# Kernel tuning notes

Measured on AMD Instinct MI355X. Metric: run time of the kernel, lower is better.

Reference implementation:

```python
import jax, jax.numpy as jnp
import numpy as np

B, L, DIM, HEADS = 4, 1024, 512, 8
HD = DIM // HEADS
HID = max(64, DIM // 2)
WIN = 32
SPARSITY = 0.3
TEMP = 1.0
PAT_TAU = 0.5


def setup_inputs() -> dict:
    key = jax.random.key(0)
    ks = jax.random.split(key, 8)
    gn = lambda k, shape, sc: jax.random.normal(k, shape, jnp.float32) * sc
    return {
        "x": jax.random.normal(ks[0], (B, L, DIM), jnp.float32),
        "mask": jnp.ones((B, L), jnp.int32),
        "Wqkv": gn(ks[1], (3 * DIM, DIM), 0.02),
        "Wproj": gn(ks[2], (DIM, DIM), 0.02),
        "bproj": jnp.zeros((DIM,), jnp.float32),
        "Wsel1": gn(ks[3], (HID, DIM), 0.05),
        "bsel1": jnp.zeros((HID,), jnp.float32),
        "Wsel2": gn(ks[4], (3, HID), 0.05),
        "bsel2": jnp.zeros((3,), jnp.float32),
        "log_pattern_tau": jnp.asarray(np.log(PAT_TAU), jnp.float32),
        "sparse_w": gn(ks[5], (HEADS,), 0.2),
        "sparse_b": jnp.zeros((HEADS,), jnp.float32),
    }


def reference(x, mask, Wqkv, Wproj, bproj, Wsel1, bsel1, Wsel2, bsel2,
              log_pattern_tau, sparse_w, sparse_b):
    Bq, Lq, D = x.shape
    scale = HD ** -0.5
    qkv = (x @ Wqkv.T).reshape(Bq, Lq, 3, HEADS, HD)
    q = jnp.transpose(qkv[:, :, 0], (0, 2, 1, 3))  # (B,H,L,hd)
    k = jnp.transpose(qkv[:, :, 1], (0, 2, 1, 3))
    v = jnp.transpose(qkv[:, :, 2], (0, 2, 1, 3))
    scores = jnp.einsum('bhid,bhjd->bhij', q, k) * scale  # (B,H,L,L)

    # pattern selector on mean-pooled features (eval: no gumbel, no dropout)
    pooled = x.mean(axis=1)
    logits = jax.nn.relu(pooled @ Wsel1.T + bsel1) @ Wsel2.T + bsel2  # (B,3)
    tau = jnp.clip(jnp.exp(log_pattern_tau), 1e-4, 10.0)
    pw = jax.nn.softmax(logits / tau, axis=-1)  # (B,3)

    half = WIN // 2
    ii = jnp.arange(Lq)[:, None]
    jj = jnp.arange(Lq)[None, :]
    local = ((jj >= ii - half) & (jj <= ii + half)).astype(jnp.float32)

    # learned sparse top-k mask per head via kth-value threshold
    kk = max(1, int(Lq * (1.0 - SPARSITY)))
    s = scores * sparse_w[None, :, None, None] + sparse_b[None, :, None, None]
    kth = jax.lax.top_k(s, kk)[0][..., -1:]
    smask = (s >= kth).astype(jnp.float32)  # (B,H,L,L)

    combined = (pw[:, 0, None, None, None] * local[None, None]
                + pw[:, 1, None, None, None]
                + pw[:, 2, None, None, None] * smask)
    neg = jnp.float32(-1e9)
    scores = jnp.where(combined > 0.05, scores, neg)
    scores = jnp.where(mask[:, None, None, :] == 0, neg, scores)

    # fallback: if a row is fully masked, unmask position 0
    all_masked = jnp.all(scores <= neg + 1e-6, axis=-1)  # (B,H,L)
    scores = scores.at[..., 0].set(jnp.where(all_masked, 0.0, scores[..., 0]))

    attn = jax.nn.softmax(scores / TEMP, axis=-1)
    out = jnp.einsum('bhij,bhjd->bhid', attn, v)
    out = jnp.transpose(out, (0, 2, 1, 3)).reshape(Bq, Lq, D)
    return out @ Wproj.T + bproj
```

## Files before the change

### kernel.cpp

```cpp
#include <hip/hip_runtime.h>
#include <math.h>

typedef __attribute__((ext_vector_type(8))) short short8;
typedef __attribute__((ext_vector_type(4))) float floatx4;

#define MFMA16(a, b, c) __builtin_amdgcn_mfma_f32_16x16x32_bf16(a, b, c, 0, 0, 0)


#define FRAG512(row, k) (((size_t)((row) >> 4)) * 8192 + (((k) >> 5) * 512) + \
                         ((((k) >> 3) & 3) * 128) + (((row) & 15) * 8) + ((k) & 7))
#define FRAGQK(row, e)  (((size_t)((row) >> 4)) * 1024 + (((e) >> 5) * 512) + \
                         ((((e) >> 3) & 3) * 128) + (((row) & 15) * 8) + ((e) & 7))

#define OFF_XB    ((size_t)0)
#define OFF_WQKV  ((size_t)4194304)
#define OFF_WPROJ ((size_t)5767168)
#define OFF_Q     ((size_t)6291456)
#define OFF_K     ((size_t)10485760)
#define OFF_VT    ((size_t)14680064)
#define OFF_AT    ((size_t)18874368)
#define OFF_PW    ((size_t)23068672)
#define OFF_PAR   ((size_t)23069696)

__device__ __forceinline__ unsigned short f2bf(float f) {
    unsigned u = __float_as_uint(f);
    return (unsigned short)((u + 0x7fffu + ((u >> 16) & 1u)) >> 16);
}
__device__ __forceinline__ float bf2f(unsigned short s) {
    return __uint_as_float((unsigned)s << 16);
}

__device__ __forceinline__ void frag_cvt_tile(const float* __restrict__ src,
                                              unsigned short* __restrict__ dst,
                                              const int t, const float sc)
{
    const int ln = t & 15, quad = (t >> 4) & 3, kh = t >> 6;
    #pragma unroll
    for (int i = 0; i < 4; ++i) {
        const int kb = kh + i * 4;
        const float* s = src + (size_t)ln * 512 + kb * 32 + quad * 8;
        float4 f0 = *(const float4*)s;
        float4 f1 = *(const float4*)(s + 4);
        unsigned short o[8] = { f2bf(f0.x * sc), f2bf(f0.y * sc), f2bf(f0.z * sc), f2bf(f0.w * sc),
                                f2bf(f1.x * sc), f2bf(f1.y * sc), f2bf(f1.z * sc), f2bf(f1.w * sc) };
        unsigned short* d = dst + kb * 512 + (size_t)(t & 63) * 8;
        *(ushort4*)d       = make_ushort4(o[0], o[1], o[2], o[3]);
        *(ushort4*)(d + 4) = make_ushort4(o[4], o[5], o[6], o[7]);
    }
}

__global__ __launch_bounds__(256)
void cvt_all(const float* __restrict__ x, const float* __restrict__ wqkv,
             const float* __restrict__ wproj, unsigned short* __restrict__ xb,
             unsigned short* __restrict__ oq, unsigned short* __restrict__ op,
             float* __restrict__ partial)
{
    const int bid = blockIdx.x, t = threadIdx.x;
    if (bid < 256) {
        const int b = bid >> 6, lb = bid & 63;
        const size_t base = ((size_t)b * 1024 + lb * 16) * 512;
        float s0 = 0.f, s1 = 0.f;
        #pragma unroll 4
        for (int l = 0; l < 16; ++l) {
            s0 += x[base + (size_t)l * 512 + t];
            s1 += x[base + (size_t)l * 512 + t + 256];
        }
        partial[((size_t)b * 64 + lb) * 512 + t] = s0;
        partial[((size_t)b * 64 + lb) * 512 + t + 256] = s1;
    } else if (bid < 512) {
        const int rt = bid - 256;
        frag_cvt_tile(x + (size_t)rt * 16 * 512, xb + (size_t)rt * 8192, t, 1.f);
    } else {
        const int tile = bid - 512;
        if (tile < 96)
            frag_cvt_tile(wqkv + (size_t)tile * 16 * 512, oq + (size_t)tile * 8192, t, 1.f);
        else
            frag_cvt_tile(wproj + (size_t)(tile - 96) * 16 * 512,
                          op + (size_t)(tile - 96) * 8192, t, 1.f);
    }
}

__global__ __launch_bounds__(128)
void gemm_qkv_sel(const unsigned short* __restrict__ xb, const unsigned short* __restrict__ wb,
                  unsigned short* __restrict__ qo, unsigned short* __restrict__ ko,
                  unsigned short* __restrict__ vo,
                  const float* __restrict__ partial, const float* __restrict__ W1,
                  const float* __restrict__ b1, const float* __restrict__ W2,
                  const float* __restrict__ b2, const float* __restrict__ ltau,
                  float* __restrict__ pwout)
{
    __shared__ __align__(16) unsigned short tile[2][64 * 72];
    const int bx = blockIdx.x, by = blockIdx.y;
    const int t = threadIdx.x;

    if (by == 64) {
        if (bx >= 4) return;
        float* pooled = (float*)&tile[0][0];
        float* h1 = pooled + 512;
        float* lg = h1 + 256;
        const int b = bx;
        #pragma unroll
        for (int c = 0; c < 4; ++c) {
            const int col = t + c * 128;
            float s = 0.f;
            for (int p = 0; p < 64; ++p) s += partial[((size_t)b * 64 + p) * 512 + col];
            pooled[col] = s * (1.f / 1024.f);
        }
        __syncthreads();
        for (int r = t; r < 256; r += 128) {
            float acc = b1[r];
            const float* w1 = W1 + (size_t)r * 512;
            for (int d = 0; d < 512; d += 4) {
                float4 w4 = *(const float4*)(w1 + d);
                acc += w4.x * pooled[d] + w4.y * pooled[d + 1] +
                       w4.z * pooled[d + 2] + w4.w * pooled[d + 3];
            }
            h1[r] = fmaxf(acc, 0.f);
        }
        __syncthreads();
        if (t < 3) {
            float a = b2[t];
            const float* w2 = W2 + t * 256;
            for (int i = 0; i < 256; ++i) a += w2[i] * h1[i];
            float tauv = fminf(fmaxf(expf(ltau[0]), 1e-4f), 10.f);
            lg[t] = a / tauv;
        }
        __syncthreads();
        if (t == 0) {
            float m = fmaxf(lg[0], fmaxf(lg[1], lg[2]));
            float e0 = expf(lg[0] - m), e1 = expf(lg[1] - m), e2 = expf(lg[2] - m);
            float inv = 1.f / (e0 + e1 + e2);
            pwout[b * 3 + 0] = e0 * inv;
            pwout[b * 3 + 1] = e1 * inv;
            pwout[b * 3 + 2] = e2 * inv;
        }
        return;
    }

    const int w = t >> 6, l64 = t & 63;
    const int ln = l64 & 15, quad = l64 >> 4;
    const int m0 = by << 6;
    const int nb0 = (bx << 7) + (w << 6);

    const unsigned short* Abase = xb + ((size_t)(m0 >> 4)) * 8192 + l64 * 8;
    const unsigned short* Bbase = wb + ((size_t)(nb0 >> 4)) * 8192 + l64 * 8;

    floatx4 acc[4][4];
    #pragma unroll
    for (int i = 0; i < 4; ++i)
        #pragma unroll
        for (int j = 0; j < 4; ++j) acc[i][j] = (floatx4){0.f, 0.f, 0.f, 0.f};

    short8 a0[4], b0[4], a1[4], b1v[4];
    #pragma unroll
    for (int i = 0; i < 4; ++i) {
        a0[i] = *(const short8*)(Abase + (size_t)i * 8192);
        b0[i] = *(const short8*)(Bbase + (size_t)i * 8192);
    }
    for (int s = 0; s < 16; s += 2) {
        #pragma unroll
        for (int i = 0; i < 4; ++i) {
            a1v: ;
            a1[i]  = *(const short8*)(Abase + (size_t)i * 8192 + (s + 1) * 512);
            b1v[i] = *(const short8*)(Bbase + (size_t)i * 8192 + (s + 1) * 512);
        }
        #pragma unroll
        for (int i = 0; i < 4; ++i)
            #pragma unroll
            for (int j = 0; j < 4; ++j)
                acc[i][j] = MFMA16(a0[i], b0[j], acc[i][j]);
        if (s + 2 < 16) {
            #pragma unroll
            for (int i = 0; i < 4; ++i) {
                a0[i] = *(const short8*)(Abase + (size_t)i * 8192 + (s + 2) * 512);
                b0[i] = *(const short8*)(Bbase + (size_t)i * 8192 + (s + 2) * 512);
            }
        }
        #pragma unroll
        for (int i = 0; i < 4; ++i)
            #pragma unroll
            for (int j = 0; j < 4; ++j)
                acc[i][j] = MFMA16(a1[i], b1v[j], acc[i][j]);
    }

    unsigned short* tw = &tile[w][0];
    const int which = bx >> 2;
    const int hh = (nb0 >> 6) & 7;
    const int g = (by >> 4) * 8 + hh;
    const int lrow0 = m0 & 1023;

    if (which == 2) {
        #pragma unroll
        for (int j = 0; j < 4; ++j)
            #pragma unroll
            for (int i = 0; i < 4; ++i)
                #pragma unroll
                for (int reg = 0; reg < 4; ++reg)
                    tw[(j * 16 + ln) * 72 + i * 16 + quad * 4 + reg] = f2bf(acc[i][j][reg]);
        const int chunk = lrow0 >> 7;
        const int ks0 = (lrow0 & 127) >> 5;
        unsigned short* dst = vo + (size_t)g * 65536 + (size_t)chunk * 8192;
        #pragma unroll
        for (int et = 0; et < 4; ++et)
            #pragma unroll
            for (int ksl = 0; ksl < 2; ++ksl) {
                const unsigned short* srcp = &tw[(et * 16 + ln) * 72 + ksl * 32 + quad * 8];
                *(short8*)(dst + (et * 4 + ks0 + ksl) * 512 + l64 * 8) = *(const short8*)srcp;
            }
    } else {
        const float sc = (which == 0) ? 0.125f : 1.f;
        #pragma unroll
        for (int j = 0; j < 4; ++j)
            #pragma unroll
            for (int i = 0; i < 4; ++i)
                #pragma unroll
                for (int reg = 0; reg < 4; ++reg)
                    tw[(i * 16 + quad * 4 + reg) * 72 + j * 16 + ln] = f2bf(acc[i][j][reg] * sc);
        unsigned short* dst = (which == 0 ? qo : ko) + (size_t)g * 65536;
        #pragma unroll
        for (int rt = 0; rt < 4; ++rt)
            #pragma unroll
            for (int eh = 0; eh < 2; ++eh) {
                const unsigned short* srcp = &tw[(rt * 16 + ln) * 72 + eh * 32 + quad * 8];
                *(short8*)(dst + ((size_t)((lrow0 >> 4) + rt)) * 1024 + eh * 512 + l64 * 8) =
                    *(const short8*)srcp;
            }
    }
}

__global__ __launch_bounds__(64)
void gemm_proj(const unsigned short* __restrict__ ab, const unsigned short* __restrict__ wb,
               const float* __restrict__ bias, float* __restrict__ out)
{
    const int t = threadIdx.x;
    const int ln = t & 15, quad = t >> 4;
    const int n0 = blockIdx.x << 6, m0 = blockIdx.y << 6;

    const unsigned short* Abase = ab + ((size_t)(m0 >> 4)) * 8192 + t * 8;
    const unsigned short* Bbase = wb + ((size_t)(n0 >> 4)) * 8192 + t * 8;

    floatx4 acc[4][4];
    #pragma unroll
    for (int i = 0; i < 4; ++i)
        #pragma unroll
        for (int j = 0; j < 4; ++j) acc[i][j] = (floatx4){0.f, 0.f, 0.f, 0.f};

    short8 a0[4], b0[4], a1[4], b1v[4];
    #pragma unroll
    for (int i = 0; i < 4; ++i) {
        a0[i] = *(const short8*)(Abase + (size_t)i * 8192);
        b0[i] = *(const short8*)(Bbase + (size_t)i * 8192);
    }
    for (int s = 0; s < 16; s += 2) {
        #pragma unroll
        for (int i = 0; i < 4; ++i) {
            a1[i]  = *(const short8*)(Abase + (size_t)i * 8192 + (s + 1) * 512);
            b1v[i] = *(const short8*)(Bbase + (size_t)i * 8192 + (s + 1) * 512);
        }
        #pragma unroll
        for (int i = 0; i < 4; ++i)
            #pragma unroll
            for (int j = 0; j < 4; ++j)
                acc[i][j] = MFMA16(a0[i], b0[j], acc[i][j]);
        if (s + 2 < 16) {
            #pragma unroll
            for (int i = 0; i < 4; ++i) {
                a0[i] = *(const short8*)(Abase + (size_t)i * 8192 + (s + 2) * 512);
                b0[i] = *(const short8*)(Bbase + (size_t)i * 8192 + (s + 2) * 512);
            }
        }
        #pragma unroll
        for (int i = 0; i < 4; ++i)
            #pragma unroll
            for (int j = 0; j < 4; ++j)
                acc[i][j] = MFMA16(a1[i], b1v[j], acc[i][j]);
    }
    #pragma unroll
    for (int j = 0; j < 4; ++j) {
        const float bv = bias[n0 + j * 16 + ln];
        #pragma unroll
        for (int i = 0; i < 4; ++i)
            #pragma unroll
            for (int reg = 0; reg < 4; ++reg)
                out[(size_t)(m0 + i * 16 + quad * 4 + reg) * 512 + n0 + j * 16 + ln] =
                    acc[i][j][reg] + bv;
    }
}

__global__ __launch_bounds__(256)
void attn_mfma(const unsigned short* __restrict__ qm, const unsigned short* __restrict__ km,
               const unsigned short* __restrict__ vm, const int* __restrict__ mask,
               const float* __restrict__ pw, const float* __restrict__ sw,
               const float* __restrict__ sb, unsigned short* __restrict__ aout)
{
    __shared__ int mk[1024];
    __shared__ float PO[4][16][68];
    __shared__ float msh[4][16], lsh[4][16];
    __shared__ unsigned kths[4][16];

    const int t = threadIdx.x;
    const int w = t >> 6, l64 = t & 63;
    const int ln = l64 & 15, quad = l64 >> 4;
    const int g = blockIdx.x & 31;
    const int rt = blockIdx.x >> 5;
    const int b = g >> 3, h = g & 7;
    const int i0 = rt * 16;

    const unsigned short* qg = qm + (size_t)g * 65536;
    const unsigned short* kg = km + (size_t)g * 65536;
    const unsigned short* vg = vm + (size_t)g * 65536;

    *(int4*)&mk[t * 4] = *(const int4*)(mask + b * 1024 + t * 4);

    const float pw0 = pw[b * 3 + 0], pw1 = pw[b * 3 + 1], pw2 = pw[b * 3 + 2];
    const bool a00 = pw1 > 0.05f;
    const bool a10 = (pw0 * 1.0f + pw1) > 0.05f;
    const bool a01 = (pw1 + pw2) > 0.05f;
    const bool a11 = ((pw0 * 1.0f + pw1) + pw2) > 0.05f;
    const bool need_sparse = (!a00 && a01) || (!a10 && a11);
    const bool flat_ok = (!need_sparse) && a00 && a10;
    const float w_h = sw[h], b_h = sb[h];
    __syncthreads();

    unsigned kth_r[4] = {0u, 0u, 0u, 0u};
    if (need_sparse) {
        unsigned* ub = (unsigned*)&PO[w][0][0];
        for (int r = 0; r < 16; ++r) {
            for (int c = 0; c < 16; ++c) {
                const int col = c * 64 + l64;
                float s = 0.f;
                for (int e = 0; e < 64; ++e)
                    s += bf2f(qg[FRAGQK(i0 + r, e)]) * bf2f(kg[FRAGQK(col, e)]);
                unsigned uu = __float_as_uint(s * w_h + b_h);
                ub[col] = (uu & 0x80000000u) ? ~uu : (uu | 0x80000000u);
            }
            unsigned u[16];
            #pragma unroll
            for (int c = 0; c < 16; ++c) u[c] = ub[l64 + c * 64];
            unsigned act = 0xFFFFu, p = 0u;
            int kk = 716;
            for (int bit = 31; bit >= 0; --bit) {
                unsigned ones = 0u;
                #pragma unroll
                for (int c = 0; c < 16; ++c)
                    if (((act >> c) & 1u) && ((u[c] >> bit) & 1u)) ones |= (1u << c);
                int c1 = __popc(ones);
                for (int off = 32; off; off >>= 1) c1 += __shfl_xor(c1, off);
                if (kk <= c1) { p |= (1u << bit); act &= ones; }
                else          { kk -= c1; act &= ~ones; }
            }
            if (l64 == 0) kths[w][r] = p;
        }
        #pragma unroll
        for (int reg = 0; reg < 4; ++reg) kth_r[reg] = kths[w][quad * 4 + reg];
    }

    const short8 aq0 = *(const short8*)(qg + ((size_t)(i0 >> 4)) * 1024 + l64 * 8);
    const short8 aq1 = *(const short8*)(qg + ((size_t)(i0 >> 4)) * 1024 + 512 + l64 * 8);

    float m_r[4] = {-3e38f, -3e38f, -3e38f, -3e38f};
    float l_r[4] = {0.f, 0.f, 0.f, 0.f};
    floatx4 accv[4];
    #pragma unroll
    for (int et = 0; et < 4; ++et) accv[et] = (floatx4){0.f, 0.f, 0.f, 0.f};
    unsigned short* Pw = (unsigned short*)&PO[w][0][0];

    #pragma unroll
    for (int cc = 0; cc < 2; ++cc) {
        const int j0 = (w * 2 + cc) << 7;
        const bool mall = __all((mk[j0 + l64] != 0) && (mk[j0 + 64 + l64] != 0));
        const bool fast = flat_ok && mall;

        const unsigned short* kbase = kg + ((size_t)(j0 >> 4)) * 1024 + l64 * 8;
        short8 kb0[8], kb1[8];
        #pragma unroll
        for (int nt = 0; nt < 8; ++nt) {
            kb0[nt] = *(const short8*)(kbase + nt * 1024);
            kb1[nt] = *(const short8*)(kbase + nt * 1024 + 512);
        }
        const unsigned short* vbase = vg + ((size_t)(j0 >> 7)) * 8192 + l64 * 8;
        short8 vb_cur[4], vb_nxt[4];
        #pragma unroll
        for (int ks = 0; ks < 4; ++ks)
            vb_cur[ks] = *(const short8*)(vbase + ks * 512);

        floatx4 sfr[8];
        #pragma unroll
        for (int nt = 0; nt < 8; ++nt) {
            floatx4 z = (floatx4){0.f, 0.f, 0.f, 0.f};
            z = MFMA16(aq0, kb0[nt], z);
            z = MFMA16(aq1, kb1[nt], z);
            sfr[nt] = z;
        }

        float rm[4] = {-3e38f, -3e38f, -3e38f, -3e38f};
        if (fast) {
            #pragma unroll
            for (int nt = 0; nt < 8; ++nt)
                #pragma unroll
                for (int reg = 0; reg < 4; ++reg) rm[reg] = fmaxf(rm[reg], sfr[nt][reg]);
        } else {
            #pragma unroll
            for (int nt = 0; nt < 8; ++nt) {
                const int j = j0 + nt * 16 + ln;
                const bool mk0 = (mk[j] == 0);
                #pragma unroll
                for (int reg = 0; reg < 4; ++reg) {
                    const int i = i0 + quad * 4 + reg;
                    const float s = sfr[nt][reg];
                    const bool loc = (j >= i - 16) && (j <= i + 16);
                    bool sm = false;
                    if (need_sparse) {
                        unsigned uu = __float_as_uint(s * w_h + b_h);
                        unsigned key = (uu & 0x80000000u) ? ~uu : (uu | 0x80000000u);
                        sm = key >= kth_r[reg];
                    }
                    bool allowed = loc ? (sm ? a11 : a10) : (sm ? a01 : a00);
                    if (mk0) allowed = false;
                    const float se = allowed ? s : -1e9f;
                    sfr[nt][reg] = se;
                    rm[reg] = fmaxf(rm[reg], se);
                }
            }
        }
        #pragma unroll
        for (int reg = 0; reg < 4; ++reg) {
            float v = rm[reg];
            v = fmaxf(v, __shfl_xor(v, 1));
            v = fmaxf(v, __shfl_xor(v, 2));
            v = fmaxf(v, __shfl_xor(v, 4));
            v = fmaxf(v, __shfl_xor(v, 8));
            rm[reg] = v;
        }
        float alpha[4], rs[4];
        #pragma unroll
        for (int reg = 0; reg < 4; ++reg) {
            const float mn = fmaxf(m_r[reg], rm[reg]);
            alpha[reg] = __expf(m_r[reg] - mn);
            m_r[reg] = mn;
            rs[reg] = 0.f;
        }
        #pragma unroll
        for (int nt = 0; nt < 8; ++nt)
            #pragma unroll
            for (int reg = 0; reg < 4; ++reg) {
                const float p = __expf(sfr[nt][reg] - m_r[reg]);
                rs[reg] += p;
                Pw[(quad * 4 + reg) * 136 + nt * 16 + ln] = f2bf(p);
            }
        #pragma unroll
        for (int reg = 0; reg < 4; ++reg) {
            float v = rs[reg];
            v += __shfl_xor(v, 1);
            v += __shfl_xor(v, 2);
            v += __shfl_xor(v, 4);
            v += __shfl_xor(v, 8);
            l_r[reg] = l_r[reg] * alpha[reg] + v;
        }
        short8 pa[4];
        #pragma unroll
        for (int ks = 0; ks < 4; ++ks)
            pa[ks] = *(const short8*)&Pw[ln * 136 + ks * 32 + quad * 8];
        #pragma unroll
        for (int et = 0; et < 4; ++et) {
            if (et < 3) {
                #pragma unroll
                for (int ks = 0; ks < 4; ++ks)
                    vb_nxt[ks] = *(const short8*)(vbase + ((et + 1) * 4 + ks) * 512);
            }
            floatx4 a = accv[et];
            a[0] *= alpha[0]; a[1] *= alpha[1]; a[2] *= alpha[2]; a[3] *= alpha[3];
            #pragma unroll
            for (int ks = 0; ks < 4; ++ks) a = MFMA16(pa[ks], vb_cur[ks], a);
            accv[et] = a;
            #pragma unroll
            for (int ks = 0; ks < 4; ++ks) vb_cur[ks] = vb_nxt[ks];
        }
    }

    #pragma unroll
    for (int et = 0; et < 4; ++et)
        #pragma unroll
        for (int reg = 0; reg < 4; ++reg)
            PO[w][quad * 4 + reg][et * 16 + ln] = accv[et][reg];
    if (ln == 0) {
        #pragma unroll
        for (int reg = 0; reg < 4; ++reg) {
            msh[w][quad * 4 + reg] = m_r[reg];
            lsh[w][quad * 4 + reg] = l_r[reg];
        }
    }
    __syncthreads();

    {
        const int r = t >> 4, cb = (t & 15) * 4;
        float M = fmaxf(fmaxf(msh[0][r], msh[1][r]), fmaxf(msh[2][r], msh[3][r]));
        float L = 0.f;
        float4 o = make_float4(0.f, 0.f, 0.f, 0.f);
        #pragma unroll
        for (int wv = 0; wv < 4; ++wv) {
            const float sc = __expf(msh[wv][r] - M);
            L += lsh[wv][r] * sc;
            float4 ov = *(const float4*)&PO[wv][r][cb];
            o.x += ov.x * sc; o.y += ov.y * sc; o.z += ov.z * sc; o.w += ov.w * sc;
        }
        ushort4 res;
        if (M <= -1e9f + 1e-6f) {
            res.x = vg[((cb + 0) >> 4) * 2048 + ((cb + 0) & 15) * 8];
            res.y = vg[((cb + 1) >> 4) * 2048 + ((cb + 1) & 15) * 8];
            res.z = vg[((cb + 2) >> 4) * 2048 + ((cb + 2) & 15) * 8];
            res.w = vg[((cb + 3) >> 4) * 2048 + ((cb + 3) & 15) * 8];
        } else {
            const float inv = 1.f / L;
            res.x = f2bf(o.x * inv); res.y = f2bf(o.y * inv);
            res.z = f2bf(o.z * inv); res.w = f2bf(o.w * inv);
        }
        const int row_g = b * 1024 + i0 + r;
        const int col = h * 64 + cb;
        *(ushort4*)&aout[FRAG512(row_g, col)] = res;
    }
}

extern "C" void kernel_launch(void* const* d_in, const int* in_sizes, int n_in,
                              void* d_out, int out_size, void* d_ws, size_t ws_size,
                              hipStream_t stream) {
    const float* x     = (const float*)d_in[0];
    const int*   mask  = (const int*)d_in[1];
    const float* Wqkv  = (const float*)d_in[2];
    const float* Wproj = (const float*)d_in[3];
    const float* bproj = (const float*)d_in[4];
    const float* Wsel1 = (const float*)d_in[5];
    const float* bsel1 = (const float*)d_in[6];
    const float* Wsel2 = (const float*)d_in[7];
    const float* bsel2 = (const float*)d_in[8];
    const float* ltau  = (const float*)d_in[9];
    const float* sw    = (const float*)d_in[10];
    const float* sb    = (const float*)d_in[11];
    char* ws = (char*)d_ws;
    unsigned short* xb     = (unsigned short*)(ws + OFF_XB);
    unsigned short* wqkvb  = (unsigned short*)(ws + OFF_WQKV);
    unsigned short* wprojb = (unsigned short*)(ws + OFF_WPROJ);
    unsigned short* q      = (unsigned short*)(ws + OFF_Q);
    unsigned short* k      = (unsigned short*)(ws + OFF_K);
    unsigned short* v      = (unsigned short*)(ws + OFF_VT);
    unsigned short* attnb  = (unsigned short*)(ws + OFF_AT);
    float* pw  = (float*)(ws + OFF_PW);
    float* par = (float*)(ws + OFF_PAR);
    float* out = (float*)d_out;
    (void)in_sizes; (void)n_in; (void)out_size; (void)ws_size;

    cvt_all<<<640, 256, 0, stream>>>(x, Wqkv, Wproj, xb, wqkvb, wprojb, par);
    gemm_qkv_sel<<<dim3(12, 65), 128, 0, stream>>>(xb, wqkvb, q, k, v,
                                                   par, Wsel1, bsel1, Wsel2, bsel2, ltau, pw);
    attn_mfma<<<2048, 256, 0, stream>>>(q, k, v, mask, pw, sw, sb, attnb);
    gemm_proj<<<dim3(8, 64), 64, 0, stream>>>(attnb, wprojb, bproj, out);
}
```

Measured before the change: 158.9 us.

## Restructure attention to share K/V tiles in LDS across four query-row waves

The attention kernel changes from four waves splitting the key range for one 16-row query tile to four waves each owning a different 16-row query tile. They share K/V chunks staged into LDS through global_load_lds, which drops the cross-wave softmax merge and cuts redundant K/V global reads. The projection GEMM is retiled to 32-row blocks to double the block count, and the selector MLP now uses wave-parallel dot products with shuffle reductions. In exchange there are per-chunk barriers and fewer attention blocks (512 instead of 2048), which could lower occupancy and latency hiding.

```diff
diff --git a/kernel.cpp b/kernel.cpp
--- a/kernel.cpp
+++ b/kernel.cpp
@@ -28,6 +28,11 @@
 }
 __device__ __forceinline__ float bf2f(unsigned short s) {
     return __uint_as_float((unsigned)s << 16);
+}
+__device__ __forceinline__ void gl16(const void* g, void* l) {
+    __builtin_amdgcn_global_load_lds(
+        (const __attribute__((address_space(1))) unsigned*)g,
+        (__attribute__((address_space(3))) unsigned*)l, 16, 0, 0);
 }
 
 __device__ __forceinline__ void frag_cvt_tile(const float* __restrict__ src,
@@ -92,13 +97,14 @@
     __shared__ __align__(16) unsigned short tile[2][64 * 72];
     const int bx = blockIdx.x, by = blockIdx.y;
     const int t = threadIdx.x;
+    const int w = t >> 6, l64 = t & 63;
 
     if (by == 64) {
         if (bx >= 4) return;
+        const int b = bx;
         float* pooled = (float*)&tile[0][0];
         float* h1 = pooled + 512;
         float* lg = h1 + 256;
-        const int b = bx;
         #pragma unroll
         for (int c = 0; c < 4; ++c) {
             const int col = t + c * 128;
@@ -107,37 +113,44 @@
             pooled[col] = s * (1.f / 1024.f);
         }
         __syncthreads();
-        for (int r = t; r < 256; r += 128) {
-            float acc = b1[r];
-            const float* w1 = W1 + (size_t)r * 512;
-            for (int d = 0; d < 512; d += 4) {
-                float4 w4 = *(const float4*)(w1 + d);
-                acc += w4.x * pooled[d] + w4.y * pooled[d + 1] +
-                       w4.z * pooled[d + 2] + w4.w * pooled[d + 3];
-            }
-            h1[r] = fmaxf(acc, 0.f);
+        for (int rr = 0; rr < 128; ++rr) {
+            const int r = w * 128 + rr;
+            const float* w1 = W1 + (size_t)r * 512 + l64 * 8;
+            float4 wa = *(const float4*)w1;
+            float4 wbv = *(const float4*)(w1 + 4);
+            const float* pd = pooled + l64 * 8;
+            float s = wa.x * pd[0] + wa.y * pd[1] + wa.z * pd[2] + wa.w * pd[3]
+                    + wbv.x * pd[4] + wbv.y * pd[5] + wbv.z * pd[6] + wbv.w * pd[7];
+            #pragma unroll
+            for (int off = 32; off; off >>= 1) s += __shfl_xor(s, off);
+            if (l64 == 0) h1[r] = fmaxf(s + b1[r], 0.f);
         }
         __syncthreads();
-        if (t < 3) {
-            float a = b2[t];
-            const float* w2 = W2 + t * 256;
-            for (int i = 0; i < 256; ++i) a += w2[i] * h1[i];
-            float tauv = fminf(fmaxf(expf(ltau[0]), 1e-4f), 10.f);
-            lg[t] = a / tauv;
-        }
-        __syncthreads();
-        if (t == 0) {
-            float m = fmaxf(lg[0], fmaxf(lg[1], lg[2]));
-            float e0 = expf(lg[0] - m), e1 = expf(lg[1] - m), e2 = expf(lg[2] - m);
-            float inv = 1.f / (e0 + e1 + e2);
-            pwout[b * 3 + 0] = e0 * inv;
-            pwout[b * 3 + 1] = e1 * inv;
-            pwout[b * 3 + 2] = e2 * inv;
+        if (w == 0) {
+            #pragma unroll
+            for (int o = 0; o < 3; ++o) {
+                float4 wv = *(const float4*)(W2 + o * 256 + l64 * 4);
+                const float* hd = h1 + l64 * 4;
+                float s = wv.x * hd[0] + wv.y * hd[1] + wv.z * hd[2] + wv.w * hd[3];
+                #pragma unroll
+                for (int off = 32; off; off >>= 1) s += __shfl_xor(s, off);
+                if (l64 == 0) {
+                    float tauv = fminf(fmaxf(expf(ltau[0]), 1e-4f), 10.f);
+                    lg[o] = (s + b2[o]) / tauv;
+                }
+            }
+            if (l64 == 0) {
+                float m = fmaxf(lg[0], fmaxf(lg[1], lg[2]));
+                float e0 = expf(lg[0] - m), e1 = expf(lg[1] - m), e2 = expf(lg[2] - m);
+                float inv = 1.f / (e0 + e1 + e2);
+                pwout[b * 3 + 0] = e0 * inv;
+                pwout[b * 3 + 1] = e1 * inv;
+                pwout[b * 3 + 2] = e2 * inv;
+            }
         }
         return;
     }
 
-    const int w = t >> 6, l64 = t & 63;
     const int ln = l64 & 15, quad = l64 >> 4;
     const int m0 = by << 6;
     const int nb0 = (bx << 7) + (w << 6);
@@ -160,7 +173,6 @@
     for (int s = 0; s < 16; s += 2) {
         #pragma unroll
         for (int i = 0; i < 4; ++i) {
-            a1v: ;
             a1[i]  = *(const short8*)(Abase + (size_t)i * 8192 + (s + 1) * 512);
             b1v[i] = *(const short8*)(Bbase + (size_t)i * 8192 + (s + 1) * 512);
         }
@@ -234,43 +246,40 @@
 {
     const int t = threadIdx.x;
     const int ln = t & 15, quad = t >> 4;
-    const int n0 = blockIdx.x << 6, m0 = blockIdx.y << 6;
+    const int n0 = blockIdx.x << 6, m0 = blockIdx.y << 5;
 
     const unsigned short* Abase = ab + ((size_t)(m0 >> 4)) * 8192 + t * 8;
     const unsigned short* Bbase = wb + ((size_t)(n0 >> 4)) * 8192 + t * 8;
 
-    floatx4 acc[4][4];
-    #pragma unroll
-    for (int i = 0; i < 4; ++i)
+    floatx4 acc[2][4];
+    #pragma unroll
+    for (int i = 0; i < 2; ++i)
         #pragma unroll
         for (int j = 0; j < 4; ++j) acc[i][j] = (floatx4){0.f, 0.f, 0.f, 0.f};
 
-    short8 a0[4], b0[4], a1[4], b1v[4];
-    #pragma unroll
-    for (int i = 0; i < 4; ++i) {
-        a0[i] = *(const short8*)(Abase + (size_t)i * 8192);
-        b0[i] = *(const short8*)(Bbase + (size_t)i * 8192);
-    }
+    short8 a0[2], b0[4], a1[2], b1v[4];
+    #pragma unroll
+    for (int i = 0; i < 2; ++i) a0[i] = *(const short8*)(Abase + (size_t)i * 8192);
+    #pragma unroll
+    for (int j = 0; j < 4; ++j) b0[j] = *(const short8*)(Bbase + (size_t)j * 8192);
     for (int s = 0; s < 16; s += 2) {
         #pragma unroll
-        for (int i = 0; i < 4; ++i) {
-            a1[i]  = *(const short8*)(Abase + (size_t)i * 8192 + (s + 1) * 512);
-            b1v[i] = *(const short8*)(Bbase + (size_t)i * 8192 + (s + 1) * 512);
-        }
-        #pragma unroll
-        for (int i = 0; i < 4; ++i)
+        for (int i = 0; i < 2; ++i) a1[i]  = *(const short8*)(Abase + (size_t)i * 8192 + (s + 1) * 512);
+        #pragma unroll
+        for (int j = 0; j < 4; ++j) b1v[j] = *(const short8*)(Bbase + (size_t)j * 8192 + (s + 1) * 512);
+        #pragma unroll
+        for (int i = 0; i < 2; ++i)
             #pragma unroll
             for (int j = 0; j < 4; ++j)
                 acc[i][j] = MFMA16(a0[i], b0[j], acc[i][j]);
         if (s + 2 < 16) {
             #pragma unroll
-            for (int i = 0; i < 4; ++i) {
-                a0[i] = *(const short8*)(Abase + (size_t)i * 8192 + (s + 2) * 512);
-                b0[i] = *(const short8*)(Bbase + (size_t)i * 8192 + (s + 2) * 512);
-            }
-        }
-        #pragma unroll
-        for (int i = 0; i < 4; ++i)
+            for (int i = 0; i < 2; ++i) a0[i] = *(const short8*)(Abase + (size_t)i * 8192 + (s + 2) * 512);
+            #pragma unroll
+            for (int j = 0; j < 4; ++j) b0[j] = *(const short8*)(Bbase + (size_t)j * 8192 + (s + 2) * 512);
+        }
+        #pragma unroll
+        for (int i = 0; i < 2; ++i)
             #pragma unroll
             for (int j = 0; j < 4; ++j)
                 acc[i][j] = MFMA16(a1[i], b1v[j], acc[i][j]);
@@ -279,7 +288,7 @@
     for (int j = 0; j < 4; ++j) {
         const float bv = bias[n0 + j * 16 + ln];
         #pragma unroll
-        for (int i = 0; i < 4; ++i)
+        for (int i = 0; i < 2; ++i)
             #pragma unroll
             for (int reg = 0; reg < 4; ++reg)
                 out[(size_t)(m0 + i * 16 + quad * 4 + reg) * 512 + n0 + j * 16 + ln] =
@@ -288,23 +297,24 @@
 }
 
 __global__ __launch_bounds__(256)
-void attn_mfma(const unsigned short* __restrict__ qm, const unsigned short* __restrict__ km,
-               const unsigned short* __restrict__ vm, const int* __restrict__ mask,
-               const float* __restrict__ pw, const float* __restrict__ sw,
-               const float* __restrict__ sb, unsigned short* __restrict__ aout)
+void attn_flash(const unsigned short* __restrict__ qm, const unsigned short* __restrict__ km,
+                const unsigned short* __restrict__ vm, const int* __restrict__ mask,
+                const float* __restrict__ pw, const float* __restrict__ sw,
+                const float* __restrict__ sb, unsigned short* __restrict__ aout)
 {
     __shared__ int mk[1024];
+    __shared__ __align__(16) unsigned short Ks[8192];
+    __shared__ __align__(16) unsigned short Vs[8192];
     __shared__ float PO[4][16][68];
-    __shared__ float msh[4][16], lsh[4][16];
     __shared__ unsigned kths[4][16];
 
     const int t = threadIdx.x;
     const int w = t >> 6, l64 = t & 63;
     const int ln = l64 & 15, quad = l64 >> 4;
     const int g = blockIdx.x & 31;
-    const int rt = blockIdx.x >> 5;
+    const int rg = blockIdx.x >> 5;
     const int b = g >> 3, h = g & 7;
-    const int i0 = rt * 16;
+    const int i0 = rg * 64 + w * 16;
 
     const unsigned short* qg = qm + (size_t)g * 65536;
     const unsigned short* kg = km + (size_t)g * 65536;
@@ -365,31 +375,30 @@
     for (int et = 0; et < 4; ++et) accv[et] = (floatx4){0.f, 0.f, 0.f, 0.f};
     unsigned short* Pw = (unsigned short*)&PO[w][0][0];
 
-    #pragma unroll
-    for (int cc = 0; cc < 2; ++cc) {
-        const int j0 = (w * 2 + cc) << 7;
+    for (int jc = 0; jc < 8; ++jc) {
+        const int j0 = jc << 7;
+        {
+            const unsigned short* kc = kg + (size_t)j0 * 64;
+            const unsigned short* vc = vg + ((size_t)(j0 >> 7)) * 8192;
+            #pragma unroll
+            for (int c = 0; c < 4; ++c) {
+                const int bi = w * 4 + c;
+                gl16(kc + bi * 512 + l64 * 8, (char*)Ks + bi * 1024);
+                gl16(vc + bi * 512 + l64 * 8, (char*)Vs + bi * 1024);
+            }
+        }
         const bool mall = __all((mk[j0 + l64] != 0) && (mk[j0 + 64 + l64] != 0));
         const bool fast = flat_ok && mall;
-
-        const unsigned short* kbase = kg + ((size_t)(j0 >> 4)) * 1024 + l64 * 8;
-        short8 kb0[8], kb1[8];
+        __syncthreads();
+
+        floatx4 sfr[8];
         #pragma unroll
         for (int nt = 0; nt < 8; ++nt) {
-            kb0[nt] = *(const short8*)(kbase + nt * 1024);
-            kb1[nt] = *(const short8*)(kbase + nt * 1024 + 512);
-        }
-        const unsigned short* vbase = vg + ((size_t)(j0 >> 7)) * 8192 + l64 * 8;
-        short8 vb_cur[4], vb_nxt[4];
-        #pragma unroll
-        for (int ks = 0; ks < 4; ++ks)
-            vb_cur[ks] = *(const short8*)(vbase + ks * 512);
-
-        floatx4 sfr[8];
-        #pragma unroll
-        for (int nt = 0; nt < 8; ++nt) {
+            const short8 kb0 = *(const short8*)(Ks + nt * 1024 + l64 * 8);
+            const short8 kb1 = *(const short8*)(Ks + nt * 1024 + 512 + l64 * 8);
             floatx4 z = (floatx4){0.f, 0.f, 0.f, 0.f};
-            z = MFMA16(aq0, kb0[nt], z);
-            z = MFMA16(aq1, kb1[nt], z);
+            z = MFMA16(aq0, kb0, z);
+            z = MFMA16(aq1, kb1, z);
             sfr[nt] = z;
         }
 
@@ -463,58 +472,35 @@
             pa[ks] = *(const short8*)&Pw[ln * 136 + ks * 32 + quad * 8];
         #pragma unroll
         for (int et = 0; et < 4; ++et) {
-            if (et < 3) {
-                #pragma unroll
-                for (int ks = 0; ks < 4; ++ks)
-                    vb_nxt[ks] = *(const short8*)(vbase + ((et + 1) * 4 + ks) * 512);
-            }
             floatx4 a = accv[et];
             a[0] *= alpha[0]; a[1] *= alpha[1]; a[2] *= alpha[2]; a[3] *= alpha[3];
             #pragma unroll
-            for (int ks = 0; ks < 4; ++ks) a = MFMA16(pa[ks], vb_cur[ks], a);
+            for (int ks = 0; ks < 4; ++ks) {
+                const short8 bv = *(const short8*)(Vs + (et * 4 + ks) * 512 + l64 * 8);
+                a = MFMA16(pa[ks], bv, a);
+            }
             accv[et] = a;
-            #pragma unroll
-            for (int ks = 0; ks < 4; ++ks) vb_cur[ks] = vb_nxt[ks];
-        }
+        }
+        __syncthreads();
     }
 
     #pragma unroll
     for (int et = 0; et < 4; ++et)
         #pragma unroll
-        for (int reg = 0; reg < 4; ++reg)
-            PO[w][quad * 4 + reg][et * 16 + ln] = accv[et][reg];
-    if (ln == 0) {
-        #pragma unroll
         for (int reg = 0; reg < 4; ++reg) {
-            msh[w][quad * 4 + reg] = m_r[reg];
-            lsh[w][quad * 4 + reg] = l_r[reg];
-        }
-    }
-    __syncthreads();
-
-    {
-        const int r = t >> 4, cb = (t & 15) * 4;
-        float M = fmaxf(fmaxf(msh[0][r], msh[1][r]), fmaxf(msh[2][r], msh[3][r]));
-        float L = 0.f;
-        float4 o = make_float4(0.f, 0.f, 0.f, 0.f);
-        #pragma unroll
-        for (int wv = 0; wv < 4; ++wv) {
-            const float sc = __expf(msh[wv][r] - M);
-            L += lsh[wv][r] * sc;
-            float4 ov = *(const float4*)&PO[wv][r][cb];
-            o.x += ov.x * sc; o.y += ov.y * sc; o.z += ov.z * sc; o.w += ov.w * sc;
-        }
-        ushort4 res;
-        if (M <= -1e9f + 1e-6f) {
-            res.x = vg[((cb + 0) >> 4) * 2048 + ((cb + 0) & 15) * 8];
-            res.y = vg[((cb + 1) >> 4) * 2048 + ((cb + 1) & 15) * 8];
-            res.z = vg[((cb + 2) >> 4) * 2048 + ((cb + 2) & 15) * 8];
-            res.w = vg[((cb + 3) >> 4) * 2048 + ((cb + 3) & 15) * 8];
-        } else {
-            const float inv = 1.f / L;
-            res.x = f2bf(o.x * inv); res.y = f2bf(o.y * inv);
-            res.z = f2bf(o.z * inv); res.w = f2bf(o.w * inv);
-        }
+            float val;
+            if (m_r[reg] <= -1e9f + 1e-6f)
+                val = bf2f(vg[et * 2048 + ln * 8]);
+            else
+                val = accv[et][reg] / l_r[reg];
+            PO[w][quad * 4 + reg][et * 16 + ln] = val;
+        }
+    #pragma unroll
+    for (int rr = 0; rr < 4; ++rr) {
+        const int r = (l64 >> 4) * 4 + rr;
+        const int cb = (l64 & 15) * 4;
+        float4 ov = *(const float4*)&PO[w][r][cb];
+        ushort4 res = make_ushort4(f2bf(ov.x), f2bf(ov.y), f2bf(ov.z), f2bf(ov.w));
         const int row_g = b * 1024 + i0 + r;
         const int col = h * 64 + cb;
         *(ushort4*)&aout[FRAG512(row_g, col)] = res;
@@ -552,6 +538,6 @@
     cvt_all<<<640, 256, 0, stream>>>(x, Wqkv, Wproj, xb, wqkvb, wprojb, par);
     gemm_qkv_sel<<<dim3(12, 65), 128, 0, stream>>>(xb, wqkvb, q, k, v,
                                                    par, Wsel1, bsel1, Wsel2, bsel2, ltau, pw);
-    attn_mfma<<<2048, 256, 0, stream>>>(q, k, v, mask, pw, sw, sb, attnb);
-    gemm_proj<<<dim3(8, 64), 64, 0, stream>>>(attnb, wprojb, bproj, out);
-}
+    attn_flash<<<512, 256, 0, stream>>>(q, k, v, mask, pw, sw, sb, attnb);
+    gemm_proj<<<dim3(8, 128), 64, 0, stream>>>(attnb, wprojb, bproj, out);
+}
```

Result: slower. 209.1 us (+31.6%).
